# Performance work log

Measured on AMD Instinct MI355X. Metric: run time of the kernel, lower is better.

Reference implementation:

```python
import jax, jax.numpy as jnp
import numpy as np

B, T, C = 4, 2048, 2048
N_HEAD = 16
HEAD_DIM = C // N_HEAD


def rotate_half(x):
    # interleaved rotate: pairs (x0,x1),(x2,x3),... -> (-x1,x0),(-x3,x2),...
    x1 = x[..., ::2]
    x2 = x[..., 1::2]
    return jnp.stack((-x2, x1), axis=-1).reshape(x.shape)


def compute_rope(seq_len, head_dim, dtype):
    inv_freq = 1.0 / (10000.0 ** (jnp.arange(0, head_dim, 2, dtype=jnp.float32) / head_dim))
    t = jnp.arange(seq_len, dtype=jnp.float32)
    freqs = t[:, None] * inv_freq[None, :]            # [T, head_dim/2]
    emb = jnp.concatenate((freqs, freqs), axis=-1)    # [T, head_dim] (module cats freqs twice)
    cos = jnp.cos(emb)[None, None, :, :].astype(dtype)
    sin = jnp.sin(emb)[None, None, :, :].astype(dtype)
    return cos, sin


def setup_inputs() -> dict:
    key = jax.random.key(0)
    k1, k2, k3, k4, k5 = jax.random.split(key, 5)
    s = 1.0 / np.sqrt(C)
    return {
        "x": jax.random.normal(k1, (B, T, C), dtype=jnp.float32),
        "Wqkv": jax.random.normal(k2, (C, 3 * C), dtype=jnp.float32) * s,
        "bqkv": jnp.zeros((3 * C,), dtype=jnp.float32),
        "Wproj": jax.random.normal(k3, (C, C), dtype=jnp.float32) * s,
        "bproj": jnp.zeros((C,), dtype=jnp.float32),
    }


def reference(x, Wqkv, bqkv, Wproj, bproj):
    Bx, Tx, Cx = x.shape
    qkv = x @ Wqkv + bqkv                              # [B,T,3C]
    q, k, v = jnp.split(qkv, 3, axis=2)
    # -> [B, H, T, D]
    q = q.reshape(Bx, Tx, N_HEAD, HEAD_DIM).transpose(0, 2, 1, 3)
    k = k.reshape(Bx, Tx, N_HEAD, HEAD_DIM).transpose(0, 2, 1, 3)
    v = v.reshape(Bx, Tx, N_HEAD, HEAD_DIM).transpose(0, 2, 1, 3)
    cos, sin = compute_rope(Tx, HEAD_DIM, x.dtype)
    q = q * cos + rotate_half(q) * sin
    k = k * cos + rotate_half(k) * sin
    scale = 1.0 / jnp.sqrt(jnp.asarray(HEAD_DIM, x.dtype))
    scores = jnp.einsum('bhqd,bhkd->bhqk', q, k) * scale
    causal = jnp.tril(jnp.ones((Tx, Tx), dtype=bool))
    scores = jnp.where(causal[None, None, :, :], scores, jnp.asarray(-jnp.inf, x.dtype))
    attn = jax.nn.softmax(scores, axis=-1)
    y = jnp.einsum('bhqk,bhkd->bhqd', attn, v)          # [B,H,T,D]
    y = y.transpose(0, 2, 1, 3).reshape(Bx, Tx, Cx)
    return y @ Wproj + bproj
```

## Files before the change

### kernel.cpp

```cpp
#include <hip/hip_runtime.h>
#include <hip/hip_bf16.h>
#include <stdint.h>

#define DEV __device__ __forceinline__
#define WAITV(n) asm volatile("s_waitcnt vmcnt(" #n ")" ::: "memory")
#define WAITL(n) asm volatile("s_waitcnt lgkmcnt(" #n ")" ::: "memory")
#define SCHEDB __builtin_amdgcn_sched_barrier(0)

typedef __attribute__((ext_vector_type(4))) float f32x4;
typedef __attribute__((ext_vector_type(8))) short bf16x8;
typedef unsigned short u16;

constexpr int Bb = 4, Tt = 2048, Ccn = 2048, NHn = 16, HDn = 128;
constexpr int MM = Bb * Tt;
constexpr int NQKV = 3 * Ccn;
constexpr int KD = 2048;
constexpr size_t K2 = (size_t)KD * 2;
constexpr size_t HKB = 128 * K2;
constexpr float QSCALE = 0.08838834764831845f;

DEV u16 f2bf(float f) {
  __hip_bfloat16 h = __float2bfloat16(f);
  return *reinterpret_cast<u16*>(&h);
}

DEV void gl_lds16(const void* g, void* l) {
  __builtin_amdgcn_global_load_lds(
      (const __attribute__((address_space(1))) void*)g,
      (__attribute__((address_space(3))) void*)l, 16, 0, 0);
}

__global__ void k_prep(const float* __restrict__ x, u16* __restrict__ xb,
                       const float* __restrict__ Wqkv, u16* __restrict__ WqkvT,
                       const float* __restrict__ Wproj, u16* __restrict__ WprojT,
                       float* __restrict__ ct, float* __restrict__ st) {
  __shared__ u16 tile[64][72];
  const int bid = blockIdx.x, tid = threadIdx.x;
  if (bid < 1024) {
    const int n4 = (MM * Ccn) >> 2;
    for (int idx = bid * 256 + tid; idx < n4; idx += 1024 * 256) {
      float4 v = ((const float4*)x)[idx];
      ushort4 o;
      o.x = f2bf(v.x); o.y = f2bf(v.y); o.z = f2bf(v.z); o.w = f2bf(v.w);
      ((ushort4*)xb)[idx] = o;
    }
  } else if (bid < 5120) {
    const float* in; u16* out; int NC, bx, by;
    if (bid < 4096) {
      int t = bid - 1024; in = Wqkv; out = WqkvT; NC = NQKV; bx = t % 96; by = t / 96;
    } else {
      int t = bid - 4096; in = Wproj; out = WprojT; NC = Ccn; bx = t & 31; by = t >> 5;
    }
    const int R = 2048;
    int tr = by * 64, tc = bx * 64;
    int r = tid >> 2, c = (tid & 3) * 16;
    const float* src = in + (size_t)(tr + r) * NC + tc + c;
#pragma unroll
    for (int i = 0; i < 16; i++) tile[r][c + i] = f2bf(src[i]);
    __syncthreads();
    u16* dst = out + (size_t)(tc + r) * R + tr + c;
#pragma unroll
    for (int i = 0; i < 16; i++) dst[i] = tile[c + i][r];
  } else {
    int idx = (bid - 5120) * 256 + tid;
    int t = idx >> 6, j = idx & 63;
    float invf = expf(-(float)j * 0.14391157f);
    float a = (float)t * invf;
    ct[idx] = cosf(a);
    st[idx] = sinf(a);
  }
}


template <int MODE>
__global__ __launch_bounds__(512, 2) void k_gemm256(
    const u16* __restrict__ A, const u16* __restrict__ Bt,
    int Ndim, int NBX,
    const float* __restrict__ bias,
    u16* __restrict__ q_r, u16* __restrict__ k_r, u16* __restrict__ vt,
    const float* __restrict__ ctab, const float* __restrict__ stab,
    float* __restrict__ outp) {
  __shared__ __align__(16) u16 SM[65536];
  const int tid = threadIdx.x;
  const int w = tid >> 6, lane = tid & 63;
  const int l16 = lane & 15, l4 = lane >> 4;
  const int wr = w >> 2, wc = w & 3;
  const int bid = blockIdx.x, nwg = gridDim.x;
  const int swz = (bid & 7) * (nwg >> 3) + (bid >> 3);
  const int by = swz / NBX, bx = swz % NBX;
  const int m0 = by * 256, n0 = bx * 256;
  constexpr int NT = KD >> 6;
  constexpr int NIT = NT >> 1;

  const int Mx = (l16 & 7) << 4;
  const int b6 = Mx & 64;
  const int lane_lo = l16 * 128 + ((l4 * 16) ^ (Mx & 48));
  const char* const pA0 = (const char*)SM + wr * 16384 + lane_lo + b6;
  const char* const pA1 = (const char*)SM + wr * 16384 + lane_lo + (64 - b6);
  const char* const pB0 = (const char*)SM + 65536 + (wc >> 1) * 16384 + (wc & 1) * 8192 + lane_lo + b6;
  const char* const pB1 = (const char*)SM + 65536 + (wc >> 1) * 16384 + (wc & 1) * 8192 + lane_lo + (64 - b6);

  uint32_t soff[2];
#pragma unroll
  for (int i = 0; i < 2; i++) {
    int op = i * 8192 + tid * 16;
    int ol = op ^ (((op >> 7) & 7) << 4);
    int row = ol >> 7, colb = ol & 127;
    soff[i] = (uint32_t)(row * (int)K2 + colb);
  }
  const char* const Ab = (const char*)A + (size_t)m0 * K2;
  const char* const Bbp = (const char*)Bt + (size_t)n0 * K2;
  char* const dstBase = (char*)SM;

  auto stA = [&](int buf, int half, int kt) {
#pragma unroll
    for (int i = 0; i < 2; i++)
      gl_lds16(Ab + (size_t)half * HKB + (size_t)kt * 128 + soff[i],
               dstBase + buf * 32768 + half * 16384 + i * 8192 + tid * 16);
  };
  auto stB = [&](int buf, int half, int kt) {
#pragma unroll
    for (int i = 0; i < 2; i++)
      gl_lds16(Bbp + (size_t)half * HKB + (size_t)kt * 128 + soff[i],
               dstBase + 65536 + buf * 32768 + half * 16384 + i * 8192 + tid * 16);
  };

  bf16x8 af[2][2][2];
  bf16x8 bfr[4][2];
  f32x4 acc[8][4];
  const f32x4 zf = {0.f, 0.f, 0.f, 0.f};
#pragma unroll
  for (int i = 0; i < 8; i++)
#pragma unroll
    for (int j = 0; j < 4; j++) acc[i][j] = zf;

  auto rdAhalf = [&](int par, int bufsel, int ph, int ks) {
    const char* base = ks ? pA1 : pA0;
#pragma unroll
    for (int dm = 0; dm < 2; dm++)
      af[par][dm][ks] = *(const bf16x8*)(base + bufsel * 32768 + (ph * 2 + dm) * 2048);
  };
  auto rdBhalf = [&](int bufsel, int ks) {
    const char* base = ks ? pB1 : pB0;
#pragma unroll
    for (int nj = 0; nj < 4; nj++)
      bfr[nj][ks] = *(const bf16x8*)(base + bufsel * 32768 + nj * 2048);
  };
  auto mfma8 = [&](int par, int ph, int ks) {
    __builtin_amdgcn_s_setprio(1);
#pragma unroll
    for (int dm = 0; dm < 2; dm++)
#pragma unroll
      for (int nj = 0; nj < 4; nj++)
        acc[ph * 2 + dm][nj] = __builtin_amdgcn_mfma_f32_16x16x32_bf16(
            af[par][dm][ks], bfr[nj][ks], acc[ph * 2 + dm][nj], 0, 0, 0);
    __builtin_amdgcn_s_setprio(0);
  };

  stA(0, 0, 0); stA(0, 1, 0); stB(0, 0, 0); stB(0, 1, 0);
  stB(1, 0, 1); stB(1, 1, 1);
  WAITV(4);
  __builtin_amdgcn_s_barrier();
  SCHEDB;
  rdAhalf(0, 0, 0, 0);
  rdBhalf(0, 0);
  rdAhalf(0, 0, 0, 1);
  rdBhalf(0, 1);

  for (int I = 0; I < NIT - 1; ++I) {
    const int t1 = 2 * I + 1, t2 = 2 * I + 2, t3 = 2 * I + 3;
#pragma unroll
    for (int gp = 0; gp < 8; ++gp) {
      __builtin_amdgcn_s_barrier();
      SCHEDB;
      { const int ng = (gp + 1) & 7; rdAhalf((gp + 1) & 1, ng >> 2, ng & 3, 0); }
      if (gp == 0)       stA(1, 0, t1);
      else if (gp == 1)  stA(1, 1, t1);
      else if (gp == 2)  stB(0, 0, t2);
      else if (gp == 3)  stB(0, 1, t2);
      else if (gp == 4)  stA(0, 0, t2);
      else if (gp == 5)  stA(0, 1, t2);
      else if (gp == 6)  stB(1, 0, t3);
      else               stB(1, 1, t3);
      if (gp == 0 || gp == 4) { WAITL(8); } else { WAITL(4); }
      SCHEDB;
      mfma8(gp & 1, gp & 3, 0);
      if (gp == 3)      rdBhalf(1, 0);
      else if (gp == 7) rdBhalf(0, 0);
      { const int ng = (gp + 1) & 7; rdAhalf((gp + 1) & 1, ng >> 2, ng & 3, 1); }
      if (gp == 3 || gp == 7) { WAITL(8); }
      else if (gp == 0 || gp == 4) { WAITL(6); }
      else { WAITL(4); }
      SCHEDB;
      mfma8(gp & 1, gp & 3, 1);
      if (gp == 3)      { rdBhalf(1, 1); SCHEDB; }
      else if (gp == 7) { rdBhalf(0, 1); SCHEDB; }
      if (gp == 2 || gp == 6) { WAITV(2); }
    }
  }
  {
    const int t1 = 2 * (NIT - 1) + 1;
#pragma unroll
    for (int gp = 0; gp < 8; ++gp) {
      __builtin_amdgcn_s_barrier();
      SCHEDB;
      if (gp < 7) { const int ng = gp + 1; rdAhalf((gp + 1) & 1, ng >> 2, ng & 3, 0); }
      if (gp == 0)       stA(1, 0, t1);
      else if (gp == 1)  stA(1, 1, t1);
      if (gp == 0 || gp == 4) { WAITL(8); }
      else if (gp == 7) { WAITL(2); }
      else { WAITL(4); }
      SCHEDB;
      mfma8(gp & 1, gp & 3, 0);
      if (gp == 3) rdBhalf(1, 0);
      if (gp < 7) { const int ng = gp + 1; rdAhalf((gp + 1) & 1, ng >> 2, ng & 3, 1); }
      if (gp == 3) { WAITL(8); }
      else if (gp == 0 || gp == 4) { WAITL(6); }
      else if (gp == 7) { WAITL(0); }
      else { WAITL(4); }
      SCHEDB;
      mfma8(gp & 1, gp & 3, 1);
      if (gp == 3) { rdBhalf(1, 1); SCHEDB; }
      if (gp == 2) { WAITV(0); }
    }
  }

  if constexpr (MODE == 1) {
#pragma unroll
    for (int mi = 0; mi < 8; mi++) {
      const int mrow = m0 + wr * 128 + mi * 16 + l4 * 4;
#pragma unroll
      for (int nj = 0; nj < 4; nj++) {
        const int col = n0 + wc * 64 + nj * 16 + l16;
        const float bi = bias[col];
#pragma unroll
        for (int jj = 0; jj < 4; jj++)
          outp[(size_t)(mrow + jj) * Ndim + col] = acc[mi][nj][jj] + bi;
      }
    }
  } else {
#pragma unroll
    for (int mi = 0; mi < 8; mi++) {
      const int mrow = m0 + wr * 128 + mi * 16 + l4 * 4;
      const int b = mrow >> 11, t0 = mrow & 2047;
#pragma unroll
      for (int nj = 0; nj < 4; nj++) {
        const int n = n0 + wc * 64 + nj * 16 + l16;
        const float bi = bias[n];
        const int part = n >> 11;
        const int hcol = n & 2047;
        const int h = hcol >> 7, d = hcol & 127;
        const int dm = d & 63;
        if (part == 2) {
          ushort4 vv;
          vv.x = f2bf(acc[mi][nj][0] + bi);
          vv.y = f2bf(acc[mi][nj][1] + bi);
          vv.z = f2bf(acc[mi][nj][2] + bi);
          vv.w = f2bf(acc[mi][nj][3] + bi);
          *(ushort4*)(vt + (((size_t)(b * NHn + h)) * HDn + d) * Tt + t0) = vv;
        } else {
#pragma unroll
          for (int jj = 0; jj < 4; jj++) {
            const int t = t0 + jj;
            float val = acc[mi][nj][jj] + bi;
            size_t didx = (((size_t)b * NHn + h) * Tt + t) * HDn + d;
            float partner = __shfl_xor(val, 1);
            float rh = (d & 1) ? partner : -partner;
            float cs = ctab[t * 64 + dm], sn = stab[t * 64 + dm];
            float o = val * cs + rh * sn;
            if (part == 0) q_r[didx] = f2bf(o * QSCALE);
            else           k_r[didx] = f2bf(o);
          }
        }
      }
    }
  }
}

__global__ __launch_bounds__(256, 2) void k_attn(
    const u16* __restrict__ q_r, const u16* __restrict__ k_r,
    const u16* __restrict__ vt, u16* __restrict__ y) {
  __shared__ u16 Ks[2][64 * 128];
  __shared__ u16 Vs[128 * 64];
  __shared__ u16 Ps[4][32 * 72];
  const int lin = blockIdx.x;
  const int swz = (lin & 7) * 64 + (lin >> 3);
  const int qpair = swz & 7;
  const int bh = swz >> 3;
  const int tid = threadIdx.x, w = tid >> 6, lane = tid & 63;
  const int l16 = lane & 15, l4 = lane >> 4;
  const int b = bh >> 4, h = bh & 15;

  const u16* kbase = k_r + (size_t)bh * Tt * HDn;
  const u16* vbase = vt + (size_t)bh * HDn * Tt;
  const f32x4 zf = {0.f, 0.f, 0.f, 0.f};

  auto stageK = [&](int buf, int j) {
    const char* ksrc = (const char*)(kbase + (size_t)j * 64 * HDn);
#pragma unroll
    for (int i = 0; i < 4; i++) {
      int op = tid * 16 + i * 4096;
      int ol = op ^ (((op >> 8) & 7) << 4);
      gl_lds16(ksrc + ol, (char*)&Ks[buf][0] + op);
    }
  };
  auto stageV = [&](int j) {
    const char* vsrc = (const char*)(vbase + (size_t)j * 64);
#pragma unroll
    for (int i = 0; i < 4; i++) {
      int op = tid * 16 + i * 4096;
      int ol = op ^ (((op >> 7) & 7) << 4);
      int row = ol >> 7, colb = ol & 127;
      gl_lds16(vsrc + (size_t)row * (Tt * 2) + colb, (char*)Vs + op);
    }
  };

#pragma unroll
  for (int qsel = 0; qsel < 2; ++qsel) {
    const int qt = qsel ? (15 - qpair) : qpair;

    const u16* qbase = q_r + ((size_t)bh * Tt + qt * 128 + w * 32) * HDn;
    bf16x8 qf[2][4];
#pragma unroll
    for (int mi = 0; mi < 2; mi++)
#pragma unroll
      for (int kc = 0; kc < 4; kc++)
        qf[mi][kc] = *(const bf16x8*)(qbase + (size_t)(mi * 16 + l16) * HDn + kc * 32 + l4 * 8);

    f32x4 acc_o[2][8];
#pragma unroll
    for (int mi = 0; mi < 2; mi++)
#pragma unroll
      for (int nf = 0; nf < 8; nf++) acc_o[mi][nf] = zf;
    float mrow[2][4], lrow[2][4];
#pragma unroll
    for (int mi = 0; mi < 2; mi++)
#pragma unroll
      for (int jj = 0; jj < 4; jj++) { mrow[mi][jj] = -1e30f; lrow[mi][jj] = 0.f; }

    const int ntiles = 2 * qt + 2;
    stageK(0, 0);
    __syncthreads();
    int cur = 0;

    for (int j = 0; j < ntiles; ++j) {
      const bool more = (j + 1 < ntiles);
      stageV(j);
      if (more) stageK(cur ^ 1, j + 1);

      f32x4 s[2][4];
#pragma unroll
      for (int mi = 0; mi < 2; mi++)
#pragma unroll
        for (int nj = 0; nj < 4; nj++) s[mi][nj] = zf;
#pragma unroll
      for (int kc = 0; kc < 4; kc++) {
        bf16x8 kf[4];
#pragma unroll
        for (int nj = 0; nj < 4; nj++) {
          int row = nj * 16 + l16;
          kf[nj] = *(const bf16x8*)((const char*)&Ks[cur][0] + row * 256 +
                                    ((kc * 64 + l4 * 16) ^ ((row & 7) << 4)));
        }
        __builtin_amdgcn_s_setprio(1);
#pragma unroll
        for (int mi = 0; mi < 2; mi++)
#pragma unroll
          for (int nj = 0; nj < 4; nj++)
            s[mi][nj] = __builtin_amdgcn_mfma_f32_16x16x32_bf16(qf[mi][kc], kf[nj], s[mi][nj], 0, 0, 0);
        __builtin_amdgcn_s_setprio(0);
      }

      const bool diag = (j >= 2 * qt);
#pragma unroll
      for (int mi = 0; mi < 2; mi++) {
#pragma unroll
        for (int jj = 0; jj < 4; jj++) {
          if (diag) {
            const int qrow = qt * 128 + w * 32 + mi * 16 + l4 * 4 + jj;
#pragma unroll
            for (int nj = 0; nj < 4; nj++) {
              const int key = j * 64 + nj * 16 + l16;
              if (key > qrow) s[mi][nj][jj] = -1e30f;
            }
          }
          float lm = fmaxf(fmaxf(s[mi][0][jj], s[mi][1][jj]), fmaxf(s[mi][2][jj], s[mi][3][jj]));
#pragma unroll
          for (int dd = 1; dd < 16; dd <<= 1) lm = fmaxf(lm, __shfl_xor(lm, dd));
          if (lm > mrow[mi][jj]) {
            const float sc = __expf(mrow[mi][jj] - lm);
            mrow[mi][jj] = lm;
            lrow[mi][jj] *= sc;
#pragma unroll
            for (int nf = 0; nf < 8; nf++) acc_o[mi][nf][jj] *= sc;
          }
          float ps = 0.f;
#pragma unroll
          for (int nj = 0; nj < 4; nj++) {
            float p = __expf(s[mi][nj][jj] - mrow[mi][jj]);
            s[mi][nj][jj] = p;
            ps += p;
          }
#pragma unroll
          for (int dd = 1; dd < 16; dd <<= 1) ps += __shfl_xor(ps, dd);
          lrow[mi][jj] += ps;
          const int prow = mi * 16 + l4 * 4 + jj;
#pragma unroll
          for (int nj = 0; nj < 4; nj++)
            Ps[w][prow * 72 + nj * 16 + l16] = f2bf(s[mi][nj][jj]);
        }
      }

      if (more) { WAITV(4); } else { WAITV(0); }
      __builtin_amdgcn_s_barrier();

#pragma unroll
      for (int kc = 0; kc < 2; kc++) {
        bf16x8 pf[2];
#pragma unroll
        for (int mi = 0; mi < 2; mi++)
          pf[mi] = *(const bf16x8*)((const char*)&Ps[w][0] + (mi * 16 + l16) * 144 + kc * 64 + l4 * 16);
        bf16x8 vf[8];
#pragma unroll
        for (int nf = 0; nf < 8; nf++) {
          int row = nf * 16 + l16;
          vf[nf] = *(const bf16x8*)((const char*)Vs + row * 128 +
                                    ((kc * 64 + l4 * 16) ^ ((row & 7) << 4)));
        }
        __builtin_amdgcn_s_setprio(1);
#pragma unroll
        for (int nf = 0; nf < 8; nf++)
#pragma unroll
          for (int mi = 0; mi < 2; mi++)
            acc_o[mi][nf] = __builtin_amdgcn_mfma_f32_16x16x32_bf16(pf[mi], vf[nf], acc_o[mi][nf], 0, 0, 0);
        __builtin_amdgcn_s_setprio(0);
      }
      __syncthreads();
      cur ^= 1;
    }

#pragma unroll
    for (int mi = 0; mi < 2; mi++) {
#pragma unroll
      for (int jj = 0; jj < 4; jj++) {
        const float rinv = 1.f / lrow[mi][jj];
        const int t = qt * 128 + w * 32 + mi * 16 + l4 * 4 + jj;
        u16* yrow = y + ((size_t)b * Tt + t) * Ccn + h * HDn;
#pragma unroll
        for (int nf = 0; nf < 8; nf++)
          yrow[nf * 16 + l16] = f2bf(acc_o[mi][nf][jj] * rinv);
      }
    }
    __syncthreads();
  }
}


extern "C" void kernel_launch(void* const* d_in, const int* in_sizes, int n_in,
                              void* d_out, int out_size, void* d_ws, size_t ws_size,
                              hipStream_t stream) {
  const float* x     = (const float*)d_in[0];
  const float* Wqkv  = (const float*)d_in[1];
  const float* bqkv  = (const float*)d_in[2];
  const float* Wproj = (const float*)d_in[3];
  const float* bproj = (const float*)d_in[4];
  float* out = (float*)d_out;
  char* ws = (char*)d_ws;

  size_t off = 0;
  auto alloc = [&](size_t bytes) -> char* {
    char* p = ws + off;
    off += (bytes + 255) & ~(size_t)255;
    return p;
  };
  float* ctab  = (float*)alloc((size_t)Tt * 64 * sizeof(float));
  float* stab  = (float*)alloc((size_t)Tt * 64 * sizeof(float));
  u16* xb      = (u16*)alloc((size_t)MM * Ccn * 2);
  u16* WqkvT   = (u16*)alloc((size_t)NQKV * Ccn * 2);
  u16* WprojT  = (u16*)alloc((size_t)Ccn * Ccn * 2);
  u16* q_rb    = (u16*)alloc((size_t)MM * Ccn * 2);
  u16* k_rb    = (u16*)alloc((size_t)MM * Ccn * 2);
  u16* vtb     = (u16*)alloc((size_t)MM * Ccn * 2);
  u16* ybuf    = (u16*)alloc((size_t)MM * Ccn * 2);

  k_prep<<<dim3(5632), 256, 0, stream>>>(x, xb, Wqkv, WqkvT, Wproj, WprojT, ctab, stab);

  k_gemm256<0><<<dim3((MM / 256) * (NQKV / 256)), 512, 0, stream>>>(
      xb, WqkvT, NQKV, NQKV / 256, bqkv, q_rb, k_rb, vtb, ctab, stab, nullptr);

  k_attn<<<dim3(512), 256, 0, stream>>>(q_rb, k_rb, vtb, ybuf);

  k_gemm256<1><<<dim3((MM / 256) * (Ccn / 256)), 512, 0, stream>>>(
      ybuf, WprojT, Ccn, Ccn / 256, bproj, nullptr, nullptr, nullptr, nullptr, nullptr, out);
}
```

Measured before the change: 444.8 us.

## Single-buffer K via register prefetch and shrink P tile to fit three blocks per CU

Replaces the double-buffered K shared-memory tile with a single buffer. The next K tile is loaded into registers during compute and written to shared memory after the PV MFMAs. The P scratch tile drops its padding and uses an XOR swizzle instead, and launch bounds rise to three blocks per CU. Together these cut LDS per block from about 66KB to 48KB to raise occupancy, at the cost of more register pressure (possible spills under the tighter VGPR cap) and a less latency-tolerant K prefetch.

Result: slower. 988.7 us (+122.3%).

```diff
diff --git a/kernel.cpp b/kernel.cpp
--- a/kernel.cpp
+++ b/kernel.cpp
@@ -277,12 +277,12 @@
   }
 }
 
-__global__ __launch_bounds__(256, 2) void k_attn(
+__global__ __launch_bounds__(256, 3) void k_attn(
     const u16* __restrict__ q_r, const u16* __restrict__ k_r,
     const u16* __restrict__ vt, u16* __restrict__ y) {
-  __shared__ u16 Ks[2][64 * 128];
+  __shared__ u16 Ks[64 * 128];
   __shared__ u16 Vs[128 * 64];
-  __shared__ u16 Ps[4][32 * 72];
+  __shared__ u16 Ps[4][32 * 64];
   const int lin = blockIdx.x;
   const int swz = (lin & 7) * 64 + (lin >> 3);
   const int qpair = swz & 7;
@@ -295,14 +295,17 @@
   const u16* vbase = vt + (size_t)bh * HDn * Tt;
   const f32x4 zf = {0.f, 0.f, 0.f, 0.f};
 
-  auto stageK = [&](int buf, int j) {
+  int kop[4], kol[4];
+#pragma unroll
+  for (int i = 0; i < 4; i++) {
+    kop[i] = tid * 16 + i * 4096;
+    kol[i] = kop[i] ^ (((kop[i] >> 8) & 7) << 4);
+  }
+
+  auto stageK0 = [&](int j) {
     const char* ksrc = (const char*)(kbase + (size_t)j * 64 * HDn);
 #pragma unroll
-    for (int i = 0; i < 4; i++) {
-      int op = tid * 16 + i * 4096;
-      int ol = op ^ (((op >> 8) & 7) << 4);
-      gl_lds16(ksrc + ol, (char*)&Ks[buf][0] + op);
-    }
+    for (int i = 0; i < 4; i++) gl_lds16(ksrc + kol[i], (char*)Ks + kop[i]);
   };
   auto stageV = [&](int j) {
     const char* vsrc = (const char*)(vbase + (size_t)j * 64);
@@ -339,14 +342,20 @@
       for (int jj = 0; jj < 4; jj++) { mrow[mi][jj] = -1e30f; lrow[mi][jj] = 0.f; }
 
     const int ntiles = 2 * qt + 2;
-    stageK(0, 0);
+    stageK0(0);
     __syncthreads();
-    int cur = 0;
 
     for (int j = 0; j < ntiles; ++j) {
       const bool more = (j + 1 < ntiles);
       stageV(j);
-      if (more) stageK(cur ^ 1, j + 1);
+      bf16x8 kr0, kr1, kr2, kr3;
+      if (more) {
+        const char* ksrc = (const char*)(kbase + (size_t)(j + 1) * 64 * HDn);
+        kr0 = *(const bf16x8*)(ksrc + kol[0]);
+        kr1 = *(const bf16x8*)(ksrc + kol[1]);
+        kr2 = *(const bf16x8*)(ksrc + kol[2]);
+        kr3 = *(const bf16x8*)(ksrc + kol[3]);
+      }
 
       f32x4 s[2][4];
 #pragma unroll
@@ -359,7 +368,7 @@
 #pragma unroll
         for (int nj = 0; nj < 4; nj++) {
           int row = nj * 16 + l16;
-          kf[nj] = *(const bf16x8*)((const char*)&Ks[cur][0] + row * 256 +
+          kf[nj] = *(const bf16x8*)((const char*)Ks + row * 256 +
                                     ((kc * 64 + l4 * 16) ^ ((row & 7) << 4)));
         }
         __builtin_amdgcn_s_setprio(1);
@@ -406,8 +415,12 @@
           lrow[mi][jj] += ps;
           const int prow = mi * 16 + l4 * 4 + jj;
 #pragma unroll
-          for (int nj = 0; nj < 4; nj++)
-            Ps[w][prow * 72 + nj * 16 + l16] = f2bf(s[mi][nj][jj]);
+          for (int nj = 0; nj < 4; nj++) {
+            int kb2 = (nj * 16 + l16) * 2;
+            Ps[w][0] = Ps[w][0];
+            *((u16*)((char*)&Ps[w][0] + prow * 128 + (kb2 ^ ((prow & 7) << 4)))) =
+                f2bf(s[mi][nj][jj]);
+          }
         }
       }
 
@@ -418,8 +431,11 @@
       for (int kc = 0; kc < 2; kc++) {
         bf16x8 pf[2];
 #pragma unroll
-        for (int mi = 0; mi < 2; mi++)
-          pf[mi] = *(const bf16x8*)((const char*)&Ps[w][0] + (mi * 16 + l16) * 144 + kc * 64 + l4 * 16);
+        for (int mi = 0; mi < 2; mi++) {
+          int row = mi * 16 + l16;
+          pf[mi] = *(const bf16x8*)((const char*)&Ps[w][0] + row * 128 +
+                                    ((kc * 64 + l4 * 16) ^ ((row & 7) << 4)));
+        }
         bf16x8 vf[8];
 #pragma unroll
         for (int nf = 0; nf < 8; nf++) {
@@ -435,8 +451,14 @@
             acc_o[mi][nf] = __builtin_amdgcn_mfma_f32_16x16x32_bf16(pf[mi], vf[nf], acc_o[mi][nf], 0, 0, 0);
         __builtin_amdgcn_s_setprio(0);
       }
+
+      if (more) {
+        *(bf16x8*)((char*)Ks + kop[0]) = kr0;
+        *(bf16x8*)((char*)Ks + kop[1]) = kr1;
+        *(bf16x8*)((char*)Ks + kop[2]) = kr2;
+        *(bf16x8*)((char*)Ks + kop[3]) = kr3;
+      }
       __syncthreads();
-      cur ^= 1;
     }
 
 #pragma unroll
```
